# Performance work log

Hardware: AMD Instinct MI355X
Metric: run time of the kernel (lower is better)

Reference implementation:

```python
import jax, jax.numpy as jnp
import numpy as np
import math

N, S, T, D = 4, 2048, 2048, 1024

def setup_inputs() -> dict:
    key = jax.random.key(0)
    ks = jax.random.split(key, 6)
    scale = 1.0 / math.sqrt(D)
    return {
        "query": jax.random.normal(ks[0], (N, S, D), dtype=jnp.float32),
        "key": jax.random.normal(ks[1], (N, T, D), dtype=jnp.float32),
        "value": jax.random.normal(ks[2], (N, T, D), dtype=jnp.float32),
        # causal mask: 1 = attend, 0 = masked out (masked_fill where mask == 0)
        "attn_mask": jnp.tril(jnp.ones((S, T), dtype=jnp.int32)),
        "Wq": jax.random.normal(ks[3], (D, D), dtype=jnp.float32) * scale,
        "Wk": jax.random.normal(ks[4], (D, D), dtype=jnp.float32) * scale,
        "Wv": jax.random.normal(ks[5], (D, D), dtype=jnp.float32) * scale,
    }

def reference(query, key, value, attn_mask, Wq, Wk, Wv):
    # nn.Linear(bias=False): y = x @ W.T
    q = jnp.einsum('nsd,ed->nse', query, Wq)
    k = jnp.einsum('ntd,ed->nte', key, Wk)
    v = jnp.einsum('ntd,ed->nte', value, Wv)
    # scaled dot-product scores [N, S, T]
    dot = jnp.einsum('nse,nte->nst', q, k) / jnp.sqrt(jnp.asarray(D, q.dtype))
    dot = jnp.where(attn_mask == 0, -jnp.inf, dot)
    scores = jax.nn.softmax(dot, axis=-1)
    # dropout is identity in eval mode
    y = jnp.einsum('nst,nte->nse', scores, v)
    return y
```

## Files before the change

### kernel.cpp

```cpp
#include <hip/hip_runtime.h>
#include <math.h>

using u16 = unsigned short;
typedef __attribute__((ext_vector_type(8))) __bf16 bf16x8;
typedef __attribute__((ext_vector_type(4))) float f32x4;
typedef __attribute__((ext_vector_type(4))) float f4v;
typedef __attribute__((ext_vector_type(8))) u16 u16x8;

__device__ __forceinline__ u16 f2bf(float f) {
  unsigned u = __float_as_uint(f);
  u += 0x7fffu + ((u >> 16) & 1u);
  return (u16)(u >> 16);
}

__device__ __forceinline__ void gload16(const void* g, void* l) {
  __builtin_amdgcn_global_load_lds(
      (const __attribute__((address_space(1))) unsigned int*)g,
      (__attribute__((address_space(3))) unsigned int*)l, 16, 0, 0);
}

__device__ __forceinline__ f32x4 MF(bf16x8 a, bf16x8 b, f32x4 c) {
  return __builtin_amdgcn_mfma_f32_16x16x32_bf16(a, b, c, 0, 0, 0);
}

__global__ __launch_bounds__(256) void cast3_f32_bf16(
    const float* __restrict__ p0, const float* __restrict__ p1,
    const float* __restrict__ p2, u16* __restrict__ out, size_t ostride) {
  int z = blockIdx.z;
  const float* in = (z == 0) ? p0 : (z == 1) ? p1 : p2;
  size_t i = ((size_t)blockIdx.x * 256 + threadIdx.x) * 8;
  f4v a = *reinterpret_cast<const f4v*>(in + i);
  f4v b = *reinterpret_cast<const f4v*>(in + i + 4);
  u16x8 r;
  r[0] = f2bf(a[0]); r[1] = f2bf(a[1]); r[2] = f2bf(a[2]); r[3] = f2bf(a[3]);
  r[4] = f2bf(b[0]); r[5] = f2bf(b[1]); r[6] = f2bf(b[2]); r[7] = f2bf(b[3]);
  *reinterpret_cast<u16x8*>(out + z * ostride + i) = r;
}

__global__ __launch_bounds__(256) void transpose_bf16k(const u16* __restrict__ in,
                                                       u16* __restrict__ out) {
  __shared__ u16 t[64][65];
  int c0 = blockIdx.x * 64, r0 = blockIdx.y * 64;
  size_t zb = (size_t)blockIdx.z * 2048 * 1024;
  const u16* I = in + zb;
  u16* O = out + zb;
  int tx = threadIdx.x & 63, ty = threadIdx.x >> 6;
  #pragma unroll
  for (int i = 0; i < 64; i += 4)
    t[ty + i][tx] = I[(size_t)(r0 + ty + i) * 1024 + c0 + tx];
  __syncthreads();
  #pragma unroll
  for (int i = 0; i < 64; i += 4)
    O[(size_t)(c0 + ty + i) * 2048 + r0 + tx] = t[tx][ty + i];
}

__global__ __launch_bounds__(256) void proj_fused(
    const float* __restrict__ Aq, const float* __restrict__ Ak,
    const float* __restrict__ Av, const u16* __restrict__ W,
    u16* __restrict__ Qp, u16* __restrict__ Kp, u16* __restrict__ Vp) {
  int h = blockIdx.x;
  int l = (h & 7) * 192 + (h >> 3);
  int bn = l & 7;
  int bm192 = l >> 3;
  int which = bm192 >> 6;
  int bm = bm192 & 63;
  const float* Ag = ((which == 0) ? Aq : (which == 1) ? Ak : Av) +
                    (size_t)bm * 128 * 1024;
  const u16* Bg = W + (size_t)which * 1048576 + (size_t)bn * 128 * 1024;
  u16* Cg = (which == 0) ? Qp : (which == 1) ? Kp : Vp;

  __shared__ __align__(16) u16 As[2][128 * 32];
  __shared__ __align__(16) u16 Bs[2][128 * 32];

  const int tid = threadIdx.x, lane = tid & 63, wave = tid >> 6;
  const int wr = wave >> 1, wc = wave & 1;
  const int fr = lane & 15, kq = (lane >> 4) * 8;

  const int arow = tid >> 1, acol = (tid & 1) * 16;
  const float* ags = Ag + (size_t)arow * 1024 + acol;
  const int ch0 = wave, ch1 = wave + 4;
  const int e0 = ch0 * 512 + lane * 8, e1 = ch1 * 512 + lane * 8;
  const int br0 = e0 >> 5, bc0 = e0 & 31, br1 = e1 >> 5, bc1 = e1 & 31;
  const u16* b0 = Bg + (size_t)br0 * 1024 + bc0;
  const u16* b1 = Bg + (size_t)br1 * 1024 + bc1;

  f32x4 acc[4][4] = {};

  {
    f4v p0 = *(const f4v*)(ags);
    f4v p1 = *(const f4v*)(ags + 4);
    f4v p2 = *(const f4v*)(ags + 8);
    f4v p3 = *(const f4v*)(ags + 12);
    gload16(b0, &Bs[0][ch0 * 512]);
    gload16(b1, &Bs[0][ch1 * 512]);
    bf16x8 w0, w1;
    w0[0] = (__bf16)p0[0]; w0[1] = (__bf16)p0[1]; w0[2] = (__bf16)p0[2]; w0[3] = (__bf16)p0[3];
    w0[4] = (__bf16)p1[0]; w0[5] = (__bf16)p1[1]; w0[6] = (__bf16)p1[2]; w0[7] = (__bf16)p1[3];
    w1[0] = (__bf16)p2[0]; w1[1] = (__bf16)p2[1]; w1[2] = (__bf16)p2[2]; w1[3] = (__bf16)p2[3];
    w1[4] = (__bf16)p3[0]; w1[5] = (__bf16)p3[1]; w1[6] = (__bf16)p3[2]; w1[7] = (__bf16)p3[3];
    *(bf16x8*)&As[0][arow * 32 + acol] = w0;
    *(bf16x8*)&As[0][arow * 32 + acol + 8] = w1;
  }
  __syncthreads();

  for (int t = 0; t < 32; ++t) {
    const int cur = t & 1;
    f4v p0, p1, p2, p3;
    if (t + 1 < 32) {
      const float* ap = ags + (t + 1) * 32;
      p0 = *(const f4v*)(ap);
      p1 = *(const f4v*)(ap + 4);
      p2 = *(const f4v*)(ap + 8);
      p3 = *(const f4v*)(ap + 12);
      const int k0 = (t + 1) * 32;
      gload16(b0 + k0, &Bs[cur ^ 1][ch0 * 512]);
      gload16(b1 + k0, &Bs[cur ^ 1][ch1 * 512]);
    }
    bf16x8 af[4], bfv[4];
    #pragma unroll
    for (int m = 0; m < 4; ++m)
      af[m] = *reinterpret_cast<const bf16x8*>(&As[cur][(wr * 64 + m * 16 + fr) * 32 + kq]);
    #pragma unroll
    for (int n = 0; n < 4; ++n)
      bfv[n] = *reinterpret_cast<const bf16x8*>(&Bs[cur][(wc * 64 + n * 16 + fr) * 32 + kq]);
    #pragma unroll
    for (int m = 0; m < 4; ++m)
      #pragma unroll
      for (int n = 0; n < 4; ++n)
        acc[m][n] = MF(af[m], bfv[n], acc[m][n]);
    if (t + 1 < 32) {
      bf16x8 w0, w1;
      w0[0] = (__bf16)p0[0]; w0[1] = (__bf16)p0[1]; w0[2] = (__bf16)p0[2]; w0[3] = (__bf16)p0[3];
      w0[4] = (__bf16)p1[0]; w0[5] = (__bf16)p1[1]; w0[6] = (__bf16)p1[2]; w0[7] = (__bf16)p1[3];
      w1[0] = (__bf16)p2[0]; w1[1] = (__bf16)p2[1]; w1[2] = (__bf16)p2[2]; w1[3] = (__bf16)p2[3];
      w1[4] = (__bf16)p3[0]; w1[5] = (__bf16)p3[1]; w1[6] = (__bf16)p3[2]; w1[7] = (__bf16)p3[3];
      *(bf16x8*)&As[cur ^ 1][arow * 32 + acol] = w0;
      *(bf16x8*)&As[cur ^ 1][arow * 32 + acol + 8] = w1;
    }
    __syncthreads();
  }

  const int row0 = bm * 128 + wr * 64 + (lane >> 4) * 4;
  const int col0 = bn * 128 + wc * 64 + fr;
  #pragma unroll
  for (int m = 0; m < 4; ++m)
    #pragma unroll
    for (int n = 0; n < 4; ++n)
      #pragma unroll
      for (int j = 0; j < 4; ++j)
        Cg[(size_t)(row0 + m * 16 + j) * 1024 + (col0 + n * 16)] = f2bf(acc[m][n][j]);
}

#define BM 128
#define BN 128
#define BK 32

template<typename OutT, int MODE>
__global__ __launch_bounds__(256) void gemm_bt(
    const u16* __restrict__ A, const u16* __restrict__ B, OutT* __restrict__ C,
    int K, int lda, int ldb, int ldc,
    size_t sA, size_t sB, size_t sC, float alpha) {
  int bn, bm, bz;
  int kEnd = K;
  if (MODE == 1) {
    int h = blockIdx.x;
    int l = (h & 7) * 68 + (h >> 3);
    bz = l / 136;
    int t = l % 136;
    bm = (int)((sqrtf(8.f * (float)t + 1.f) - 1.f) * 0.5f);
    while ((bm + 1) * (bm + 2) / 2 <= t) ++bm;
    while (bm * (bm + 1) / 2 > t) --bm;
    bn = t - bm * (bm + 1) / 2;
  } else {
    int l = blockIdx.x;
    bm = 15 - (l >> 5);
    int rest = l & 31;
    bz = rest >> 3;
    bn = rest & 7;
    kEnd = (K < (bm + 1) * BM) ? K : (bm + 1) * BM;
  }
  const u16* Ag = A + sA * bz + (size_t)bm * BM * lda;
  const u16* Bg = B + sB * bz + (size_t)bn * BN * ldb;
  OutT* Cg = C + sC * bz;

  __shared__ __align__(16) u16 As[2][BM * BK];
  __shared__ __align__(16) u16 Bs[2][BN * BK];

  const int tid = threadIdx.x;
  const int lane = tid & 63, wave = tid >> 6;
  const int wr = wave >> 1, wc = wave & 1;

  const int ch0 = wave, ch1 = wave + 4;
  const int e0 = ch0 * 512 + lane * 8, e1 = ch1 * 512 + lane * 8;
  const int r0 = e0 >> 5, c0 = e0 & 31, r1 = e1 >> 5, c1 = e1 & 31;
  const u16* a0 = Ag + (size_t)r0 * lda + c0;
  const u16* a1 = Ag + (size_t)r1 * lda + c1;
  const u16* b0 = Bg + (size_t)r0 * ldb + c0;
  const u16* b1 = Bg + (size_t)r1 * ldb + c1;

  f32x4 acc[4][4] = {};

  const int fr = lane & 15, kq = (lane >> 4) * 8;
  const int nt = kEnd / BK;

  gload16(a0, &As[0][ch0 * 512]);
  gload16(a1, &As[0][ch1 * 512]);
  gload16(b0, &Bs[0][ch0 * 512]);
  gload16(b1, &Bs[0][ch1 * 512]);
  __syncthreads();

  for (int t = 0; t < nt; ++t) {
    const int cur = t & 1;
    if (t + 1 < nt) {
      const int k0 = (t + 1) * BK;
      gload16(a0 + k0, &As[cur ^ 1][ch0 * 512]);
      gload16(a1 + k0, &As[cur ^ 1][ch1 * 512]);
      gload16(b0 + k0, &Bs[cur ^ 1][ch0 * 512]);
      gload16(b1 + k0, &Bs[cur ^ 1][ch1 * 512]);
    }
    bf16x8 af[4], bfv[4];
    #pragma unroll
    for (int m = 0; m < 4; ++m)
      af[m] = *reinterpret_cast<const bf16x8*>(&As[cur][(wr * 64 + m * 16 + fr) * BK + kq]);
    #pragma unroll
    for (int n = 0; n < 4; ++n)
      bfv[n] = *reinterpret_cast<const bf16x8*>(&Bs[cur][(wc * 64 + n * 16 + fr) * BK + kq]);
    #pragma unroll
    for (int m = 0; m < 4; ++m)
      #pragma unroll
      for (int n = 0; n < 4; ++n)
        acc[m][n] = MF(af[m], bfv[n], acc[m][n]);
    __syncthreads();
  }

  const int row0 = bm * BM + wr * 64 + (lane >> 4) * 4;
  const int col0 = bn * BN + wc * 64 + fr;
  #pragma unroll
  for (int m = 0; m < 4; ++m)
    #pragma unroll
    for (int n = 0; n < 4; ++n) {
      #pragma unroll
      for (int j = 0; j < 4; ++j) {
        float val = acc[m][n][j] * alpha;
        size_t idx = (size_t)(row0 + m * 16 + j) * ldc + (col0 + n * 16);
        if constexpr (sizeof(OutT) == 2) Cg[idx] = f2bf(val);
        else Cg[idx] = val;
      }
    }
}

__global__ __launch_bounds__(256) void softmax_causal(float* __restrict__ sc) {
  int r = blockIdx.x;
  int s = r & 2047;
  float* row = sc + (size_t)r * 2048;
  int tid = threadIdx.x;
  int t0 = tid * 8;
  f4v x0 = {-1e30f, -1e30f, -1e30f, -1e30f};
  f4v x1 = {-1e30f, -1e30f, -1e30f, -1e30f};
  if (t0 <= s)     x0 = reinterpret_cast<const f4v*>(row)[tid * 2];
  if (t0 + 4 <= s) x1 = reinterpret_cast<const f4v*>(row)[tid * 2 + 1];
  float v[8] = {x0[0], x0[1], x0[2], x0[3], x1[0], x1[1], x1[2], x1[3]};
  float mx = -1e30f;
  #pragma unroll
  for (int j = 0; j < 8; ++j) {
    v[j] = ((t0 + j) <= s) ? v[j] : -1e30f;
    mx = fmaxf(mx, v[j]);
  }
  #pragma unroll
  for (int o = 32; o; o >>= 1) mx = fmaxf(mx, __shfl_xor(mx, o, 64));
  __shared__ float red[8];
  if ((tid & 63) == 0) red[tid >> 6] = mx;
  __syncthreads();
  mx = fmaxf(fmaxf(red[0], red[1]), fmaxf(red[2], red[3]));
  float p[8];
  float sum = 0.f;
  #pragma unroll
  for (int j = 0; j < 8; ++j) {
    p[j] = ((t0 + j) <= s) ? __expf(v[j] - mx) : 0.f;
    sum += p[j];
  }
  #pragma unroll
  for (int o = 32; o; o >>= 1) sum += __shfl_xor(sum, o, 64);
  if ((tid & 63) == 0) red[4 + (tid >> 6)] = sum;
  __syncthreads();
  sum = red[4] + red[5] + red[6] + red[7];
  float inv = 1.0f / sum;
  u16x8 o8;
  #pragma unroll
  for (int j = 0; j < 8; ++j) o8[j] = f2bf(p[j] * inv);
  if (t0 <= (s | 127))
    reinterpret_cast<u16x8*>(row)[tid] = o8;
}

extern "C" void kernel_launch(void* const* d_in, const int* in_sizes, int n_in,
                              void* d_out, int out_size, void* d_ws, size_t ws_size,
                              hipStream_t stream) {
  const float* q  = (const float*)d_in[0];
  const float* k  = (const float*)d_in[1];
  const float* v  = (const float*)d_in[2];
  const float* Wq = (const float*)d_in[4];
  const float* Wk = (const float*)d_in[5];
  const float* Wv = (const float*)d_in[6];
  float* out = (float*)d_out;
  char* ws = (char*)d_ws;

  const size_t MB = 1024ull * 1024ull;
  float* sc = (float*)ws;
  u16* Vp  = (u16*)(ws + 0 * MB);
  u16* wqb = (u16*)(ws + 16 * MB);
  u16* Vt  = (u16*)(ws + 64 * MB);
  u16* Kp  = (u16*)(ws + 80 * MB);
  u16* Qp  = (u16*)(ws + 96 * MB);
  (void)in_sizes; (void)n_in; (void)out_size; (void)ws_size;

  cast3_f32_bf16<<<dim3(512, 1, 3), 256, 0, stream>>>(Wq, Wk, Wv, wqb, 1048576);

  proj_fused<<<1536, 256, 0, stream>>>(q, k, v, wqb, Qp, Kp, Vp);

  transpose_bf16k<<<dim3(16, 32, 4), 256, 0, stream>>>(Vp, Vt);

  gemm_bt<float, 1><<<544, 256, 0, stream>>>(
      Qp, Kp, sc, 1024, 1024, 1024, 2048,
      (size_t)2048 * 1024, (size_t)2048 * 1024, (size_t)2048 * 2048, 0.03125f);

  softmax_causal<<<8192, 256, 0, stream>>>(sc);

  gemm_bt<float, 2><<<512, 256, 0, stream>>>(
      (u16*)ws, Vt, out, 2048, 4096, 2048, 1024,
      (size_t)2048 * 4096, (size_t)1024 * 2048, (size_t)2048 * 1024, 1.0f);
}
```

Baseline: 186.0 us.

## Prefetch fp32 A tiles two stages ahead with manual waitcnt barriers in QKV projection

The projection GEMM now loads the fp32 activation tile two K-steps ahead in registers, while B still goes to LDS one step ahead. Each thread's A load is remapped to rows tid>>2 and tid>>2+64, 8 floats each. The __syncthreads is replaced by explicit s_waitcnt vmcnt(4)/lgkmcnt(0) plus s_barrier, so outstanding register loads are not drained at each barrier. The goal is to hide global latency better, at the cost of more registers and fragile hand-counted vmcnt values.

```diff
diff --git a/kernel.cpp b/kernel.cpp
--- a/kernel.cpp
+++ b/kernel.cpp
@@ -21,6 +21,13 @@
 
 __device__ __forceinline__ f32x4 MF(bf16x8 a, bf16x8 b, f32x4 c) {
   return __builtin_amdgcn_mfma_f32_16x16x32_bf16(a, b, c, 0, 0, 0);
+}
+
+__device__ __forceinline__ bf16x8 pk8(f4v a, f4v b) {
+  bf16x8 x;
+  x[0] = (__bf16)a[0]; x[1] = (__bf16)a[1]; x[2] = (__bf16)a[2]; x[3] = (__bf16)a[3];
+  x[4] = (__bf16)b[0]; x[5] = (__bf16)b[1]; x[6] = (__bf16)b[2]; x[7] = (__bf16)b[3];
+  return x;
 }
 
 __global__ __launch_bounds__(256) void cast3_f32_bf16(
@@ -76,8 +83,10 @@
   const int wr = wave >> 1, wc = wave & 1;
   const int fr = lane & 15, kq = (lane >> 4) * 8;
 
-  const int arow = tid >> 1, acol = (tid & 1) * 16;
-  const float* ags = Ag + (size_t)arow * 1024 + acol;
+  const float* ag0 = Ag + (size_t)(tid >> 2) * 1024 + (tid & 3) * 8;
+  const float* ag1 = ag0 + 64 * 1024;
+  const int w0i = (tid >> 2) * 32 + (tid & 3) * 8;
+  const int w1i = w0i + 2048;
   const int ch0 = wave, ch1 = wave + 4;
   const int e0 = ch0 * 512 + lane * 8, e1 = ch1 * 512 + lane * 8;
   const int br0 = e0 >> 5, bc0 = e0 & 31, br1 = e1 >> 5, bc1 = e1 & 31;
@@ -85,36 +94,33 @@
   const u16* b1 = Bg + (size_t)br1 * 1024 + bc1;
 
   f32x4 acc[4][4] = {};
-
-  {
-    f4v p0 = *(const f4v*)(ags);
-    f4v p1 = *(const f4v*)(ags + 4);
-    f4v p2 = *(const f4v*)(ags + 8);
-    f4v p3 = *(const f4v*)(ags + 12);
-    gload16(b0, &Bs[0][ch0 * 512]);
-    gload16(b1, &Bs[0][ch1 * 512]);
-    bf16x8 w0, w1;
-    w0[0] = (__bf16)p0[0]; w0[1] = (__bf16)p0[1]; w0[2] = (__bf16)p0[2]; w0[3] = (__bf16)p0[3];
-    w0[4] = (__bf16)p1[0]; w0[5] = (__bf16)p1[1]; w0[6] = (__bf16)p1[2]; w0[7] = (__bf16)p1[3];
-    w1[0] = (__bf16)p2[0]; w1[1] = (__bf16)p2[1]; w1[2] = (__bf16)p2[2]; w1[3] = (__bf16)p2[3];
-    w1[4] = (__bf16)p3[0]; w1[5] = (__bf16)p3[1]; w1[6] = (__bf16)p3[2]; w1[7] = (__bf16)p3[3];
-    *(bf16x8*)&As[0][arow * 32 + acol] = w0;
-    *(bf16x8*)&As[0][arow * 32 + acol + 8] = w1;
-  }
-  __syncthreads();
+  f4v pc0, pc1, pc2, pc3, pn0, pn1, pn2, pn3;
+
+  gload16(b0, &Bs[0][ch0 * 512]);
+  gload16(b1, &Bs[0][ch1 * 512]);
+  pc0 = *(const f4v*)(ag0);      pc1 = *(const f4v*)(ag0 + 4);
+  pc2 = *(const f4v*)(ag1);      pc3 = *(const f4v*)(ag1 + 4);
+  pn0 = *(const f4v*)(ag0 + 32); pn1 = *(const f4v*)(ag0 + 36);
+  pn2 = *(const f4v*)(ag1 + 32); pn3 = *(const f4v*)(ag1 + 36);
+  *(bf16x8*)&As[0][w0i] = pk8(pc0, pc1);
+  *(bf16x8*)&As[0][w1i] = pk8(pc2, pc3);
+  pc0 = pn0; pc1 = pn1; pc2 = pn2; pc3 = pn3;
+  asm volatile("s_waitcnt vmcnt(4)" ::: "memory");
+  asm volatile("s_waitcnt lgkmcnt(0)" ::: "memory");
+  __builtin_amdgcn_s_barrier();
 
   for (int t = 0; t < 32; ++t) {
     const int cur = t & 1;
-    f4v p0, p1, p2, p3;
-    if (t + 1 < 32) {
-      const float* ap = ags + (t + 1) * 32;
-      p0 = *(const f4v*)(ap);
-      p1 = *(const f4v*)(ap + 4);
-      p2 = *(const f4v*)(ap + 8);
-      p3 = *(const f4v*)(ap + 12);
+    if (t < 31) {
       const int k0 = (t + 1) * 32;
       gload16(b0 + k0, &Bs[cur ^ 1][ch0 * 512]);
       gload16(b1 + k0, &Bs[cur ^ 1][ch1 * 512]);
+    }
+    if (t < 30) {
+      const float* ap0 = ag0 + (t + 2) * 32;
+      const float* ap1 = ag1 + (t + 2) * 32;
+      pn0 = *(const f4v*)(ap0); pn1 = *(const f4v*)(ap0 + 4);
+      pn2 = *(const f4v*)(ap1); pn3 = *(const f4v*)(ap1 + 4);
     }
     bf16x8 af[4], bfv[4];
     #pragma unroll
@@ -128,16 +134,15 @@
       #pragma unroll
       for (int n = 0; n < 4; ++n)
         acc[m][n] = MF(af[m], bfv[n], acc[m][n]);
-    if (t + 1 < 32) {
-      bf16x8 w0, w1;
-      w0[0] = (__bf16)p0[0]; w0[1] = (__bf16)p0[1]; w0[2] = (__bf16)p0[2]; w0[3] = (__bf16)p0[3];
-      w0[4] = (__bf16)p1[0]; w0[5] = (__bf16)p1[1]; w0[6] = (__bf16)p1[2]; w0[7] = (__bf16)p1[3];
-      w1[0] = (__bf16)p2[0]; w1[1] = (__bf16)p2[1]; w1[2] = (__bf16)p2[2]; w1[3] = (__bf16)p2[3];
-      w1[4] = (__bf16)p3[0]; w1[5] = (__bf16)p3[1]; w1[6] = (__bf16)p3[2]; w1[7] = (__bf16)p3[3];
-      *(bf16x8*)&As[cur ^ 1][arow * 32 + acol] = w0;
-      *(bf16x8*)&As[cur ^ 1][arow * 32 + acol + 8] = w1;
-    }
-    __syncthreads();
+    if (t < 31) {
+      *(bf16x8*)&As[cur ^ 1][w0i] = pk8(pc0, pc1);
+      *(bf16x8*)&As[cur ^ 1][w1i] = pk8(pc2, pc3);
+      pc0 = pn0; pc1 = pn1; pc2 = pn2; pc3 = pn3;
+      if (t < 30) { asm volatile("s_waitcnt vmcnt(4)" ::: "memory"); }
+      else        { asm volatile("s_waitcnt vmcnt(0)" ::: "memory"); }
+      asm volatile("s_waitcnt lgkmcnt(0)" ::: "memory");
+      __builtin_amdgcn_s_barrier();
+    }
   }
 
   const int row0 = bm * 128 + wr * 64 + (lane >> 4) * 4;
```

After: 180.7 us. 1.03x faster.
